# Kernel tuning notes

Hardware: AMD Instinct MI355X
Metric: run time of the kernel (lower is better)

## Reference

```python
import jax, jax.numpy as jnp
import numpy as np

B, M, D = 512, 100000, 256
EPS = 1e-8  # torch.cosine_similarity eps
TEMP = 10.0  # softmax temperature from source


def setup_inputs() -> dict:
    key = jax.random.key(0)
    kx, kk, kv = jax.random.split(key, 3)
    x = jax.random.normal(kx, (B, D), dtype=jnp.float32)
    memory_keys = jax.random.normal(kk, (M, D), dtype=jnp.float32) * 0.1
    memory_values = jax.random.normal(kv, (M, D), dtype=jnp.float32) * 0.1
    return {"x": x, "memory_keys": memory_keys, "memory_values": memory_values}


def reference(x, memory_keys, memory_values):
    # cosine similarity between x [B,D] and memory_keys [M,D] -> [B,M]
    dots = jnp.einsum("bd,md->bm", x, memory_keys)
    xn = jnp.linalg.norm(x, axis=-1)          # [B]
    kn = jnp.linalg.norm(memory_keys, axis=-1)  # [M]
    denom = jnp.maximum(xn[:, None] * kn[None, :], EPS)
    sims = dots / denom                         # [B,M]
    attn = jax.nn.softmax(sims * TEMP, axis=-1)  # [B,M]
    retrieved = jnp.einsum("bm,md->bd", attn, memory_values)  # [B,D]
    return retrieved, attn
```

## Files before the change

### kernel.cpp

```cpp
#include <hip/hip_runtime.h>
#include <hip/hip_bf16.h>


#define MCOLS 100000
#define MP    100032
#define DDIM  256
#define CHUNK 1792
#define NTFULL 28
#define NCHUNK 56
#define NSLOT 56
#define CHUNK1 832
#define NT1   26
#define NCH1  128
#define ATTN_OFF 131072
#define WS_RXN  0
#define WS_RKN  512
#define WS_RCPL 100512
#define WS_XB_BYTE   409600ull
#define WS_VT_BYTE   1048576ull
#define WS_PART_BYTE 52264960ull
#define WS_KB_BYTE   84246528ull
#define WS_KB_END    (WS_KB_BYTE + 2ull*(size_t)MCOLS*DDIM)

#define GLL(g, l) __builtin_amdgcn_global_load_lds( \
    (const __attribute__((address_space(1))) void*)(g), \
    (__attribute__((address_space(3))) void*)(l), 16, 0, 0)

typedef short short8 __attribute__((ext_vector_type(8)));
typedef float f32x4  __attribute__((ext_vector_type(4)));

static __device__ __forceinline__ unsigned short f2bfu(float f) {
  union { __hip_bfloat16 h; unsigned short u; } cv;
  cv.h = __float2bfloat16(f);
  return cv.u;
}
static __device__ __forceinline__ unsigned int pk2(float a, float b) {
  return (unsigned int)f2bfu(a) | ((unsigned int)f2bfu(b) << 16);
}
static __device__ __forceinline__ short8 pack8(float4 a, float4 b) {
  short8 r;
  r[0] = (short)f2bfu(a.x); r[1] = (short)f2bfu(a.y);
  r[2] = (short)f2bfu(a.z); r[3] = (short)f2bfu(a.w);
  r[4] = (short)f2bfu(b.x); r[5] = (short)f2bfu(b.y);
  r[6] = (short)f2bfu(b.z); r[7] = (short)f2bfu(b.w);
  return r;
}

__global__ void k0_xn(const float* __restrict__ x, float* __restrict__ ws) {
  const int b = blockIdx.x, t = threadIdx.x;
  const float v = x[b*DDIM + t];
  float s = v*v;
  #pragma unroll
  for (int mk = 1; mk <= 32; mk <<= 1) s += __shfl_xor(s, mk);
  __shared__ float ps[4];
  if ((t & 63) == 0) ps[t >> 6] = s;
  __syncthreads();
  const float tot = ps[0] + ps[1] + ps[2] + ps[3];
  const float r10 = 10.0f / fmaxf(sqrtf(tot), 1e-12f);
  if (t == 0) ws[WS_RXN + b] = r10;
  unsigned short* xbp = (unsigned short*)((char*)ws + WS_XB_BYTE);
  xbp[b*DDIM + t] = f2bfu(v * r10);
}

template<bool WRITEKB>
__global__ __launch_bounds__(256) void k0c_kn(const float* __restrict__ K,
                                              float* __restrict__ ws) {
  const int t = threadIdx.x;
  const int mg = blockIdx.x*64 + (t >> 2);
  const int qq = t & 3;
  if (mg >= MCOLS) return;
  const float* kp = K + (size_t)mg*DDIM + 64*qq;
  float4 buf[16];
  float ss = 0.f;
  #pragma unroll
  for (int j = 0; j < 16; ++j) {
    buf[j] = *(const float4*)(kp + 4*j);
    ss += buf[j].x*buf[j].x + buf[j].y*buf[j].y + buf[j].z*buf[j].z + buf[j].w*buf[j].w;
  }
  ss += __shfl_xor(ss, 1); ss += __shfl_xor(ss, 2);
  const float rk = 1.0f / fmaxf(sqrtf(ss), 1e-12f);
  if (qq == 0) ws[WS_RKN + mg] = rk;
  if (WRITEKB) {
    unsigned int* kb = (unsigned int*)((char*)ws + WS_KB_BYTE);
    #pragma unroll
    for (int j = 0; j < 8; ++j) {
      const float4 a = buf[2*j], b2 = buf[2*j+1];
      uint4 u;
      u.x = pk2(a.x*rk, a.y*rk);  u.y = pk2(a.z*rk, a.w*rk);
      u.z = pk2(b2.x*rk, b2.y*rk); u.w = pk2(b2.z*rk, b2.w*rk);
      const int slot = (8*qq + j) ^ (mg & 7);
      *(uint4*)(kb + (size_t)mg*128 + slot*4) = u;
    }
  }
}

__global__ __launch_bounds__(256) void k0b_tr(const float* __restrict__ V,
                                              float* __restrict__ ws) {
  const int t = threadIdx.x;
  const int m0 = blockIdx.x * 64;
  __shared__ float vt_f[64][261];
  #pragma unroll
  for (int i = 0; i < 4; ++i) {
    const int ml = (t >> 4) + 16*i;
    const int mg = m0 + ml;
    #pragma unroll
    for (int j = 0; j < 4; ++j) {
      const int d = 4*(t & 15) + 64*j;
      float4 v = make_float4(0.f, 0.f, 0.f, 0.f);
      if (mg < MCOLS) v = *(const float4*)(V + (size_t)mg*DDIM + d);
      vt_f[ml][d] = v.x; vt_f[ml][d+1] = v.y; vt_f[ml][d+2] = v.z; vt_f[ml][d+3] = v.w;
    }
  }
  __syncthreads();
  unsigned short* vt = (unsigned short*)((char*)ws + WS_VT_BYTE);
  const int tl = t & 15;
  const int s = tl >> 1, hf = tl & 1;
  const int mq = 8*s + 4*hf;
  #pragma unroll
  for (int it = 0; it < 16; ++it) {
    const int d = (t >> 4) + 16*it;
    uint2 u;
    u.x = pk2(vt_f[mq+0][d], vt_f[mq+1][d]);
    u.y = pk2(vt_f[mq+2][d], vt_f[mq+3][d]);
    const int sp = s ^ (d & 7);
    *(uint2*)(vt + (size_t)d*MP + m0 + sp*8 + 4*hf) = u;
  }
}

static __device__ __forceinline__ void stage_k(const char* __restrict__ kb,
                                               int m0, int w, int l,
                                               unsigned short (*klds)[256]) {
  #pragma unroll
  for (int i = 0; i < 4; ++i) {
    int r = m0 + w*8 + i*2 + (l >> 5);
    r = min(r, MCOLS - 1);
    const char* g = kb + (size_t)r*512 + (l & 31)*16;
    char* dst = (char*)&klds[w*8 + i*2][0];
    GLL(g, dst);
  }
}
static __device__ __forceinline__ void stage_k32(const char* __restrict__ kb,
                                                 int m0, int w, int l,
                                                 unsigned short (*klds)[256]) {
  #pragma unroll
  for (int i = 0; i < 2; ++i) {
    int r = m0 + w*4 + i*2 + (l >> 5);
    r = min(r, MCOLS - 1);
    const char* g = kb + (size_t)r*512 + (l & 31)*16;
    char* dst = (char*)&klds[w*4 + i*2][0];
    GLL(g, dst);
  }
}
static __device__ __forceinline__ void stage_vt(const char* __restrict__ vtb,
                                                int m1, int w, int l,
                                                unsigned short (*vtl)[64]) {
  #pragma unroll
  for (int i = 0; i < 4; ++i) {
    const int d = w*32 + i*8 + (l >> 3);
    const int ms = min(m1 + (l & 7)*8, MP - 8);
    const char* g = vtb + ((size_t)d*MP + ms)*2;
    char* dst = (char*)&vtl[w*32 + i*8][0];
    GLL(g, dst);
  }
}

__global__ __launch_bounds__(512, 8) void k1b_sum(const float* __restrict__ ws,
                                                  float* __restrict__ out) {
  const int bid = blockIdx.x;
  const int xg = bid & 7, i = bid >> 3;
  const int c = xg + 8*(i & 15), rb = i >> 4;
  const int t = threadIdx.x, w = t >> 6, l = t & 63, q = l >> 4, ln = l & 15;
  const int ar = w & 3, h = w >> 2, l7 = ln & 7;
  __shared__ __align__(16) unsigned short klds2[2][32][256];
  const char* kb = (const char*)ws + WS_KB_BYTE;
  const unsigned short* xb = (const unsigned short*)((const char*)ws + WS_XB_BYTE);
  const int R0 = rb*64;

  short8 xf[8];
  {
    const int row = R0 + 16*ar + ln;
    #pragma unroll
    for (int kk = 0; kk < 8; ++kk)
      xf[kk] = *(const short8*)(xb + row*DDIM + 32*kk + 8*q);
  }
  float lpr[4] = {0.f,0.f,0.f,0.f};
  const int mbase = c*CHUNK1;
  const int rem = MCOLS - mbase;
  const int nt = rem <= 0 ? 0 : min(NT1, (rem + 31) >> 5);

  if (nt > 0) {
    stage_k32(kb, mbase, w, l, klds2[0]);
    __syncthreads();
    for (int mt = 0; mt < nt; ++mt) {
      const int cur = mt & 1;
      const int m0 = mbase + mt*32;
      if (mt + 1 < nt) stage_k32(kb, m0 + 32, w, l, klds2[cur ^ 1]);
      const char* kbase = (const char*)&klds2[cur][0][0];
      const int row0 = 16*h + ln;
      f32x4 acc = {0.f,0.f,0.f,0.f};
      #pragma unroll
      for (int kk = 0; kk < 8; ++kk) {
        const int sl = ((q + 4*kk) ^ l7) << 4;
        const short8 b0 = *(const short8*)(kbase + row0*512 + sl);
        acc = __builtin_amdgcn_mfma_f32_16x16x32_bf16(xf[kk], b0, acc, 0,0,0);
      }
      const int mr = m0 + row0;
      const bool ok = mr < MCOLS;
      #pragma unroll
      for (int r = 0; r < 4; ++r)
        lpr[r] += ok ? __expf(acc[r]) : 0.f;
      __syncthreads();
    }
  }
  #pragma unroll
  for (int r = 0; r < 4; ++r) {
    float s = lpr[r];
    s += __shfl_xor(s, 1); s += __shfl_xor(s, 2);
    s += __shfl_xor(s, 4); s += __shfl_xor(s, 8);
    if (ln == 0)
      out[(size_t)(c*2 + h)*512 + R0 + 16*ar + 4*q + r] = s;
  }
}

template<int NSUM>
__global__ void k2_final(const float* __restrict__ out, float* __restrict__ ws) {
  const int b = blockIdx.x, t = threadIdx.x;
  float v = (t < NSUM) ? out[(size_t)t*512 + b] : 0.f;
  #pragma unroll
  for (int mk = 1; mk <= 32; mk <<= 1) v += __shfl_xor(v, mk);
  __shared__ float s2[4];
  if ((t & 63) == 0) s2[t >> 6] = v;
  __syncthreads();
  if (t == 0) ws[WS_RCPL + b] = 1.0f / (s2[0] + s2[1] + s2[2] + s2[3]);
}

__global__ __launch_bounds__(512, 4) void k3a_main(float* __restrict__ ws,
                                                   float* __restrict__ out) {
  const int bid = blockIdx.x;
  const int xg = bid & 7, i = bid >> 3;
  const int c = xg + 8*(i % 7), rb = i / 7;
  const int t = threadIdx.x, w = t >> 6, l = t & 63, q = l >> 4, ln = l & 15;
  const int ar = w & 3, h = w >> 2, l7 = ln & 7;
  __shared__ __align__(16) unsigned short klds[64][256];
  __shared__ __align__(16) unsigned short vtl[256][64];
  __shared__ __align__(16) unsigned short plds[64][64];
  const char* kb  = (const char*)ws + WS_KB_BYTE;
  const char* vtb = (const char*)ws + WS_VT_BYTE;
  const unsigned short* xb = (const unsigned short*)((const char*)ws + WS_XB_BYTE);
  const int R0 = rb*64;

  short8 xf[8];
  {
    const int row = R0 + 16*ar + ln;
    #pragma unroll
    for (int kk = 0; kk < 8; ++kk)
      xf[kk] = *(const short8*)(xb + row*DDIM + 32*kk + 8*q);
  }
  float rlq[4];
  #pragma unroll
  for (int r = 0; r < 4; ++r)
    rlq[r] = ws[WS_RCPL + R0 + 16*ar + 4*q + r];
  f32x4 apv[8];
  #pragma unroll
  for (int dx = 0; dx < 8; ++dx) { f32x4 z = {0.f,0.f,0.f,0.f}; apv[dx] = z; }
  const int d2 = 128*h;
  float* attn = out + ATTN_OFF;
  const int mbase = c*CHUNK;
  const int nt = min(NTFULL, (MCOLS - mbase + 63) >> 6);
  unsigned short* pf = &plds[0][0];

  stage_k(kb, mbase, w, l, klds);
  __syncthreads();

  for (int mt = 0; mt < nt; ++mt) {
    const int m0 = mbase + mt*64;
    stage_vt(vtb, m0, w, l, vtl);
    const int row0 = 32*h + ln;
    f32x4 acc[2];
    { f32x4 z = {0.f,0.f,0.f,0.f}; acc[0] = z; acc[1] = z; }
    #pragma unroll
    for (int kk = 0; kk < 8; ++kk) {
      const int sl = ((q + 4*kk) ^ l7) << 4;
      const short8 b0 = *(const short8*)((const char*)&klds[0][0] + row0*512 + sl);
      const short8 b1 = *(const short8*)((const char*)&klds[0][0] + (row0 + 16)*512 + sl);
      acc[0] = __builtin_amdgcn_mfma_f32_16x16x32_bf16(xf[kk], b0, acc[0], 0,0,0);
      acc[1] = __builtin_amdgcn_mfma_f32_16x16x32_bf16(xf[kk], b1, acc[1], 0,0,0);
    }
    const int mr0 = m0 + row0, mr1 = mr0 + 16;
    const bool ok0 = mr0 < MCOLS, ok1 = mr1 < MCOLS;
    #pragma unroll
    for (int r = 0; r < 4; ++r) {
      const int rowl = 16*ar + 4*q + r;
      const float p0v = ok0 ? __expf(acc[0][r]) : 0.f;
      const float p1v = ok1 ? __expf(acc[1][r]) : 0.f;
      float* arow = attn + (size_t)(R0 + rowl)*MCOLS;
      if (ok0) arow[mr0] = p0v*rlq[r];
      if (ok1) arow[mr1] = p1v*rlq[r];
      const int r7 = rowl & 7;
      pf[rowl*64 + ((((ln>>3) + 4*h    ) ^ r7) << 3) + (ln & 7)] = f2bfu(p0v);
      pf[rowl*64 + ((((ln>>3) + 4*h + 2) ^ r7) << 3) + (ln & 7)] = f2bfu(p1v);
    }
    __syncthreads();
    if (mt + 1 < nt) stage_k(kb, m0 + 64, w, l, klds);
    const int prow = 16*ar + ln;
    const short8 af0 = *(const short8*)(pf + prow*64 + ((q       ^ l7) << 3));
    const short8 af1 = *(const short8*)(pf + prow*64 + (((4 + q) ^ l7) << 3));
    #pragma unroll
    for (int dx = 0; dx < 8; ++dx) {
      const int R = d2 + 16*dx + ln;
      const char* vr = (const char*)&vtl[0][0] + R*128;
      const short8 bv0 = *(const short8*)(vr + ((q       ^ l7) << 4));
      const short8 bv1 = *(const short8*)(vr + (((4 + q) ^ l7) << 4));
      apv[dx] = __builtin_amdgcn_mfma_f32_16x16x32_bf16(af0, bv0, apv[dx], 0,0,0);
      apv[dx] = __builtin_amdgcn_mfma_f32_16x16x32_bf16(af1, bv1, apv[dx], 0,0,0);
    }
    __syncthreads();
  }

  float* part = (float*)((char*)ws + WS_PART_BYTE);
  #pragma unroll
  for (int dx = 0; dx < 8; ++dx)
    #pragma unroll
    for (int r = 0; r < 4; ++r)
      part[((size_t)c*512 + R0 + 16*ar + 4*q + r)*256 + d2 + 16*dx + ln]
        = apv[dx][r]*rlq[r];
}

static __device__ __forceinline__ void load_xf(const float* __restrict__ x,
                                               int brow0, int q, int ln,
                                               short8 xf[2][8]) {
  #pragma unroll
  for (int as = 0; as < 2; ++as) {
    const int row = brow0 + 16*as + ln;
    #pragma unroll
    for (int kk = 0; kk < 8; ++kk) {
      const float* p = x + row*DDIM + 32*kk + 8*q;
      xf[as][kk] = pack8(*(const float4*)p, *(const float4*)(p + 4));
    }
  }
}

__global__ __launch_bounds__(512, 2) void k3b_main(const float* __restrict__ x,
                                                   const float* __restrict__ K,
                                                   float* __restrict__ ws,
                                                   float* __restrict__ out) {
  const int bid = blockIdx.x;
  const int c = bid >> 2, rb = bid & 3;
  const int t = threadIdx.x, w = t >> 6, l = t & 63, q = l >> 4, ln = l & 15;
  const int h = w & 1, rg = w >> 1;
  __shared__ __align__(16) unsigned short plds[2][128][72];
  const int R0 = rb*128;
  short8 xf[2][8];
  const int brow0 = R0 + 32*rg;
  load_xf(x, brow0, q, ln, xf);
  float rxn[2][4];
  #pragma unroll
  for (int as = 0; as < 2; ++as)
    #pragma unroll
    for (int r = 0; r < 4; ++r)
      rxn[as][r] = ws[WS_RXN + brow0 + 16*as + 4*q + r];
  float lpr[2][4] = {{0.f,0.f,0.f,0.f},{0.f,0.f,0.f,0.f}};
  f32x4 apv[2][8];
  #pragma unroll
  for (int bs = 0; bs < 2; ++bs)
    #pragma unroll
    for (int dx = 0; dx < 8; ++dx) { f32x4 z = {0.f,0.f,0.f,0.f}; apv[bs][dx] = z; }
  const int b2 = 32*(w & 3), d2 = 128*(w >> 2);
  const unsigned short* vt = (const unsigned short*)((const char*)ws + WS_VT_BYTE);
  const float* rknw = ws + WS_RKN;
  float* attn = out + ATTN_OFF;
  const int mbase = c*CHUNK;
  const int nt = min(NTFULL, (MCOLS - mbase + 63) >> 6);
  const int l7 = ln & 7;

  for (int mt = 0; mt < nt; ++mt) {
    const int m0 = mbase + mt*64;
    const int mr0 = m0 + 32*h + ln, mr1 = mr0 + 16;
    const int kr0 = min(mr0, MCOLS-1), kr1 = min(mr1, MCOLS-1);
    f32x4 acc[2][2];
    #pragma unroll
    for (int as = 0; as < 2; ++as)
      #pragma unroll
      for (int mm = 0; mm < 2; ++mm) { f32x4 z = {0.f,0.f,0.f,0.f}; acc[as][mm] = z; }
    const float* p0 = K + (size_t)kr0*DDIM + 8*q;
    const float* p1 = K + (size_t)kr1*DDIM + 8*q;
    #pragma unroll
    for (int kk = 0; kk < 8; ++kk) {
      const short8 b0 = pack8(*(const float4*)(p0 + 32*kk), *(const float4*)(p0 + 32*kk + 4));
      const short8 b1 = pack8(*(const float4*)(p1 + 32*kk), *(const float4*)(p1 + 32*kk + 4));
      acc[0][0] = __builtin_amdgcn_mfma_f32_16x16x32_bf16(xf[0][kk], b0, acc[0][0], 0,0,0);
      acc[0][1] = __builtin_amdgcn_mfma_f32_16x16x32_bf16(xf[0][kk], b1, acc[0][1], 0,0,0);
      acc[1][0] = __builtin_amdgcn_mfma_f32_16x16x32_bf16(xf[1][kk], b0, acc[1][0], 0,0,0);
      acc[1][1] = __builtin_amdgcn_mfma_f32_16x16x32_bf16(xf[1][kk], b1, acc[1][1], 0,0,0);
    }
    const float rk0 = rknw[kr0], rk1 = rknw[kr1];
    const bool ok0 = mr0 < MCOLS, ok1 = mr1 < MCOLS;
    #pragma unroll
    for (int as = 0; as < 2; ++as)
      #pragma unroll
      for (int r = 0; r < 4; ++r) {
        const int rowl = 32*rg + 16*as + 4*q + r;
        const float p0v = ok0 ? __expf(acc[as][0][r]*rxn[as][r]*rk0) : 0.f;
        const float p1v = ok1 ? __expf(acc[as][1][r]*rxn[as][r]*rk1) : 0.f;
        float* arow = attn + (size_t)(R0 + rowl)*MCOLS;
        if (ok0) arow[mr0] = p0v;
        if (ok1) arow[mr1] = p1v;
        lpr[as][r] += p0v + p1v;
        plds[mt & 1][rowl][32*h + ln]      = f2bfu(p0v);
        plds[mt & 1][rowl][32*h + 16 + ln] = f2bfu(p1v);
      }
    __syncthreads();
    const unsigned short (*pb)[72] = plds[mt & 1];
    const short8 af00 = *(const short8*)&pb[b2 + ln][8*q];
    const short8 af01 = *(const short8*)&pb[b2 + ln][32 + 8*q];
    const short8 af10 = *(const short8*)&pb[b2 + 16 + ln][8*q];
    const short8 af11 = *(const short8*)&pb[b2 + 16 + ln][32 + 8*q];
    #pragma unroll
    for (int dx = 0; dx < 8; ++dx) {
      const int R = d2 + 16*dx + ln;
      const size_t rbase = (size_t)R*MP + m0;
      const short8 bv0 = *(const short8*)(vt + rbase + ((q     ^ (R & 7)) << 3));
      const short8 bv1 = *(const short8*)(vt + rbase + (((4+q) ^ (R & 7)) << 3));
      apv[0][dx] = __builtin_amdgcn_mfma_f32_16x16x32_bf16(af00, bv0, apv[0][dx], 0,0,0);
      apv[0][dx] = __builtin_amdgcn_mfma_f32_16x16x32_bf16(af01, bv1, apv[0][dx], 0,0,0);
      apv[1][dx] = __builtin_amdgcn_mfma_f32_16x16x32_bf16(af10, bv0, apv[1][dx], 0,0,0);
      apv[1][dx] = __builtin_amdgcn_mfma_f32_16x16x32_bf16(af11, bv1, apv[1][dx], 0,0,0);
    }
  }

  #pragma unroll
  for (int as = 0; as < 2; ++as)
    #pragma unroll
    for (int r = 0; r < 4; ++r) {
      float s = lpr[as][r];
      s += __shfl_xor(s, 1); s += __shfl_xor(s, 2);
      s += __shfl_xor(s, 4); s += __shfl_xor(s, 8);
      if (ln == 0)
        out[(size_t)(c*2 + h)*512 + brow0 + 16*as + 4*q + r] = s;
    }
  float* part = (float*)((char*)ws + WS_PART_BYTE);
  #pragma unroll
  for (int bs = 0; bs < 2; ++bs)
    #pragma unroll
    for (int dx = 0; dx < 8; ++dx)
      #pragma unroll
      for (int r = 0; r < 4; ++r)
        part[((size_t)c*512 + R0 + b2 + 16*bs + 4*q + r)*256 + d2 + 16*dx + ln]
          = apv[bs][dx][r];
}

template<bool NORM>
__global__ void k4_red(const float* __restrict__ ws, float* __restrict__ out) {
  const int b = blockIdx.x, t = threadIdx.x;
  const float* part = (const float*)((const char*)ws + WS_PART_BYTE);
  float acc = 0.f;
  for (int cc = 0; cc < NSLOT; ++cc)
    acc += part[((size_t)cc*512 + b)*256 + t];
  if (!NORM) acc *= ws[WS_RCPL + b];
  out[b*DDIM + t] = acc;
}

__global__ void k5_scale(const float* __restrict__ ws, float* __restrict__ out) {
  const int row = blockIdx.y;
  const int i4 = blockIdx.x*256 + threadIdx.x;
  if (i4 >= MCOLS/4) return;
  const float s = ws[WS_RCPL + row];
  float4* p = (float4*)(out + ATTN_OFF + (size_t)row*MCOLS) + i4;
  float4 v = *p;
  v.x *= s; v.y *= s; v.z *= s; v.w *= s;
  *p = v;
}

extern "C" void kernel_launch(void* const* d_in, const int* in_sizes, int n_in,
                              void* d_out, int out_size, void* d_ws, size_t ws_size,
                              hipStream_t stream) {
  const float* x = (const float*)d_in[0];
  const float* K = (const float*)d_in[1];
  const float* V = (const float*)d_in[2];
  float* out = (float*)d_out;
  float* ws  = (float*)d_ws;
  const bool useKB = ws_size >= WS_KB_END;

  k0_xn<<<512, 256, 0, stream>>>(x, ws);
  if (useKB) k0c_kn<true ><<<1563, 256, 0, stream>>>(K, ws);
  else       k0c_kn<false><<<1563, 256, 0, stream>>>(K, ws);
  k0b_tr<<<MP/64, 256, 0, stream>>>(V, ws);
  if (useKB) {
    k1b_sum<<<1024, 512, 0, stream>>>(ws, out);
    k2_final<256><<<512, 256, 0, stream>>>(out, ws);
    k3a_main<<<448, 512, 0, stream>>>(ws, out);
    k4_red<true><<<512, 256, 0, stream>>>(ws, out);
  } else {
    k3b_main<<<224, 512, 0, stream>>>(x, K, ws, out);
    k2_final<112><<<512, 256, 0, stream>>>(out, ws);
    k5_scale<<<dim3((MCOLS/4 + 255)/256, 512), 256, 0, stream>>>(ws, out);
    k4_red<false><<<512, 256, 0, stream>>>(ws, out);
  }
}
```

Measured before the change: 253.1 us.

## Fuse key normalization and bf16 conversion with softmax-denominator pass

Replaces the separate key-normalize/bf16-pack kernel and the k1b_sum exp-sum kernel with one fused kernel. Each block loads 64 key rows, normalizes them, writes the bf16 keys to workspace and LDS, then runs MFMA against all 512 x rows to produce partial exp sums per chunk. This avoids rereading the bf16 keys from global memory in a separate pass and removes one launch. The cost is a larger partial-sum reduction (1563 chunks) and reloading x fragments from global for every block. In the KB path the fused kernel no longer writes the per-key reciprocal norm (WS_RKN), which the before code stored there.

```diff
diff --git a/kernel.cpp b/kernel.cpp
--- a/kernel.cpp
+++ b/kernel.cpp
@@ -9,9 +9,8 @@
 #define NTFULL 28
 #define NCHUNK 56
 #define NSLOT 56
-#define CHUNK1 832
-#define NT1   26
-#define NCH1  128
+#define NCHA  1563
+#define PSTAT_OFF 50530816
 #define ATTN_OFF 131072
 #define WS_RXN  0
 #define WS_RKN  512
@@ -62,7 +61,94 @@
   xbp[b*DDIM + t] = f2bfu(v * r10);
 }
 
-template<bool WRITEKB>
+__global__ __launch_bounds__(512, 4) void kA_fused(const float* __restrict__ K,
+                                                   float* __restrict__ ws,
+                                                   float* __restrict__ out) {
+  const int c = blockIdx.x;
+  const int m0 = c*64;
+  const int t = threadIdx.x;
+  __shared__ __align__(16) unsigned short klds[64][264];
+  {
+    const int ml = t >> 3, tc = t & 7;
+    const int mg = m0 + ml;
+    const bool mok = mg < MCOLS;
+    const float* kp = K + (size_t)(mok ? mg : MCOLS-1)*DDIM + 32*tc;
+    float4 buf[8];
+    float ss = 0.f;
+    #pragma unroll
+    for (int j = 0; j < 8; ++j) {
+      buf[j] = *(const float4*)(kp + 4*j);
+      ss += buf[j].x*buf[j].x + buf[j].y*buf[j].y + buf[j].z*buf[j].z + buf[j].w*buf[j].w;
+    }
+    ss += __shfl_xor(ss, 1); ss += __shfl_xor(ss, 2); ss += __shfl_xor(ss, 4);
+    const float rk = mok ? (1.0f / fmaxf(sqrtf(ss), 1e-12f)) : 0.f;
+    unsigned int* kb = (unsigned int*)((char*)ws + WS_KB_BYTE);
+    #pragma unroll
+    for (int j = 0; j < 4; ++j) {
+      const float4 a = buf[2*j], b2 = buf[2*j+1];
+      uint4 u;
+      u.x = pk2(a.x*rk, a.y*rk);   u.y = pk2(a.z*rk, a.w*rk);
+      u.z = pk2(b2.x*rk, b2.y*rk); u.w = pk2(b2.z*rk, b2.w*rk);
+      const int slot = 4*tc + j;
+      if (mok) *(uint4*)(kb + (size_t)mg*128 + (slot ^ (ml & 7))*4) = u;
+      *(uint4*)&klds[ml][slot*8] = u;
+    }
+  }
+  __syncthreads();
+  const int w = t >> 6, l = t & 63, q = l >> 4, ln = l & 15;
+  const unsigned short* xb = (const unsigned short*)((const char*)ws + WS_XB_BYTE);
+  float* pst = out + PSTAT_OFF + (size_t)c*512;
+  #pragma unroll 1
+  for (int as = 0; as < 4; ++as) {
+    const int xrow = 64*w + 16*as + ln;
+    short8 xf[8];
+    #pragma unroll
+    for (int kk = 0; kk < 8; ++kk)
+      xf[kk] = *(const short8*)(xb + xrow*DDIM + 32*kk + 8*q);
+    f32x4 acc[4];
+    #pragma unroll
+    for (int mm = 0; mm < 4; ++mm) { f32x4 z = {0.f,0.f,0.f,0.f}; acc[mm] = z; }
+    #pragma unroll
+    for (int kk = 0; kk < 8; ++kk) {
+      #pragma unroll
+      for (int mm = 0; mm < 4; ++mm) {
+        const short8 b = *(const short8*)((const char*)&klds[0][0]
+                                          + (16*mm + ln)*528 + (4*kk + q)*16);
+        acc[mm] = __builtin_amdgcn_mfma_f32_16x16x32_bf16(xf[kk], b, acc[mm], 0,0,0);
+      }
+    }
+    float srow[4] = {0.f, 0.f, 0.f, 0.f};
+    #pragma unroll
+    for (int mm = 0; mm < 4; ++mm) {
+      const bool ok = (m0 + 16*mm + ln) < MCOLS;
+      #pragma unroll
+      for (int r = 0; r < 4; ++r)
+        srow[r] += ok ? __expf(acc[mm][r]) : 0.f;
+    }
+    #pragma unroll
+    for (int r = 0; r < 4; ++r) {
+      float s = srow[r];
+      s += __shfl_xor(s, 1); s += __shfl_xor(s, 2);
+      s += __shfl_xor(s, 4); s += __shfl_xor(s, 8);
+      if (ln == 0) pst[64*w + 16*as + 4*q + r] = s;
+    }
+  }
+}
+
+__global__ void k2A_final(const float* __restrict__ out, float* __restrict__ ws) {
+  const int b = blockIdx.x, t = threadIdx.x;
+  const float* pst = out + PSTAT_OFF;
+  float v = 0.f;
+  for (int ch = t; ch < NCHA; ch += 256)
+    v += pst[(size_t)ch*512 + b];
+  #pragma unroll
+  for (int mk = 1; mk <= 32; mk <<= 1) v += __shfl_xor(v, mk);
+  __shared__ float s2[4];
+  if ((t & 63) == 0) s2[t >> 6] = v;
+  __syncthreads();
+  if (t == 0) ws[WS_RCPL + b] = 1.0f / (s2[0] + s2[1] + s2[2] + s2[3]);
+}
+
 __global__ __launch_bounds__(256) void k0c_kn(const float* __restrict__ K,
                                               float* __restrict__ ws) {
   const int t = threadIdx.x;
@@ -70,28 +156,14 @@
   const int qq = t & 3;
   if (mg >= MCOLS) return;
   const float* kp = K + (size_t)mg*DDIM + 64*qq;
-  float4 buf[16];
   float ss = 0.f;
   #pragma unroll
   for (int j = 0; j < 16; ++j) {
-    buf[j] = *(const float4*)(kp + 4*j);
-    ss += buf[j].x*buf[j].x + buf[j].y*buf[j].y + buf[j].z*buf[j].z + buf[j].w*buf[j].w;
+    const float4 a = *(const float4*)(kp + 4*j);
+    ss += a.x*a.x + a.y*a.y + a.z*a.z + a.w*a.w;
   }
   ss += __shfl_xor(ss, 1); ss += __shfl_xor(ss, 2);
-  const float rk = 1.0f / fmaxf(sqrtf(ss), 1e-12f);
-  if (qq == 0) ws[WS_RKN + mg] = rk;
-  if (WRITEKB) {
-    unsigned int* kb = (unsigned int*)((char*)ws + WS_KB_BYTE);
-    #pragma unroll
-    for (int j = 0; j < 8; ++j) {
-      const float4 a = buf[2*j], b2 = buf[2*j+1];
-      uint4 u;
-      u.x = pk2(a.x*rk, a.y*rk);  u.y = pk2(a.z*rk, a.w*rk);
-      u.z = pk2(b2.x*rk, b2.y*rk); u.w = pk2(b2.z*rk, b2.w*rk);
-      const int slot = (8*qq + j) ^ (mg & 7);
-      *(uint4*)(kb + (size_t)mg*128 + slot*4) = u;
-    }
-  }
+  if (qq == 0) ws[WS_RKN + mg] = 1.0f / fmaxf(sqrtf(ss), 1e-12f);
 }
 
 __global__ __launch_bounds__(256) void k0b_tr(const float* __restrict__ V,
@@ -139,18 +211,6 @@
     GLL(g, dst);
   }
 }
-static __device__ __forceinline__ void stage_k32(const char* __restrict__ kb,
-                                                 int m0, int w, int l,
-                                                 unsigned short (*klds)[256]) {
-  #pragma unroll
-  for (int i = 0; i < 2; ++i) {
-    int r = m0 + w*4 + i*2 + (l >> 5);
-    r = min(r, MCOLS - 1);
-    const char* g = kb + (size_t)r*512 + (l & 31)*16;
-    char* dst = (char*)&klds[w*4 + i*2][0];
-    GLL(g, dst);
-  }
-}
 static __device__ __forceinline__ void stage_vt(const char* __restrict__ vtb,
                                                 int m1, int w, int l,
                                                 unsigned short (*vtl)[64]) {
@@ -161,64 +221,6 @@
     const char* g = vtb + ((size_t)d*MP + ms)*2;
     char* dst = (char*)&vtl[w*32 + i*8][0];
     GLL(g, dst);
-  }
-}
-
-__global__ __launch_bounds__(512, 8) void k1b_sum(const float* __restrict__ ws,
-                                                  float* __restrict__ out) {
-  const int bid = blockIdx.x;
-  const int xg = bid & 7, i = bid >> 3;
-  const int c = xg + 8*(i & 15), rb = i >> 4;
-  const int t = threadIdx.x, w = t >> 6, l = t & 63, q = l >> 4, ln = l & 15;
-  const int ar = w & 3, h = w >> 2, l7 = ln & 7;
-  __shared__ __align__(16) unsigned short klds2[2][32][256];
-  const char* kb = (const char*)ws + WS_KB_BYTE;
-  const unsigned short* xb = (const unsigned short*)((const char*)ws + WS_XB_BYTE);
-  const int R0 = rb*64;
-
-  short8 xf[8];
-  {
-    const int row = R0 + 16*ar + ln;
-    #pragma unroll
-    for (int kk = 0; kk < 8; ++kk)
-      xf[kk] = *(const short8*)(xb + row*DDIM + 32*kk + 8*q);
-  }
-  float lpr[4] = {0.f,0.f,0.f,0.f};
-  const int mbase = c*CHUNK1;
-  const int rem = MCOLS - mbase;
-  const int nt = rem <= 0 ? 0 : min(NT1, (rem + 31) >> 5);
-
-  if (nt > 0) {
-    stage_k32(kb, mbase, w, l, klds2[0]);
-    __syncthreads();
-    for (int mt = 0; mt < nt; ++mt) {
-      const int cur = mt & 1;
-      const int m0 = mbase + mt*32;
-      if (mt + 1 < nt) stage_k32(kb, m0 + 32, w, l, klds2[cur ^ 1]);
-      const char* kbase = (const char*)&klds2[cur][0][0];
-      const int row0 = 16*h + ln;
-      f32x4 acc = {0.f,0.f,0.f,0.f};
-      #pragma unroll
-      for (int kk = 0; kk < 8; ++kk) {
-        const int sl = ((q + 4*kk) ^ l7) << 4;
-        const short8 b0 = *(const short8*)(kbase + row0*512 + sl);
-        acc = __builtin_amdgcn_mfma_f32_16x16x32_bf16(xf[kk], b0, acc, 0,0,0);
-      }
-      const int mr = m0 + row0;
-      const bool ok = mr < MCOLS;
-      #pragma unroll
-      for (int r = 0; r < 4; ++r)
-        lpr[r] += ok ? __expf(acc[r]) : 0.f;
-      __syncthreads();
-    }
-  }
-  #pragma unroll
-  for (int r = 0; r < 4; ++r) {
-    float s = lpr[r];
-    s += __shfl_xor(s, 1); s += __shfl_xor(s, 2);
-    s += __shfl_xor(s, 4); s += __shfl_xor(s, 8);
-    if (ln == 0)
-      out[(size_t)(c*2 + h)*512 + R0 + 16*ar + 4*q + r] = s;
   }
 }
 
@@ -482,15 +484,15 @@
   const bool useKB = ws_size >= WS_KB_END;
 
   k0_xn<<<512, 256, 0, stream>>>(x, ws);
-  if (useKB) k0c_kn<true ><<<1563, 256, 0, stream>>>(K, ws);
-  else       k0c_kn<false><<<1563, 256, 0, stream>>>(K, ws);
-  k0b_tr<<<MP/64, 256, 0, stream>>>(V, ws);
   if (useKB) {
-    k1b_sum<<<1024, 512, 0, stream>>>(ws, out);
-    k2_final<256><<<512, 256, 0, stream>>>(out, ws);
+    kA_fused<<<NCHA, 512, 0, stream>>>(K, ws, out);
+    k0b_tr<<<MP/64, 256, 0, stream>>>(V, ws);
+    k2A_final<<<512, 256, 0, stream>>>(out, ws);
     k3a_main<<<448, 512, 0, stream>>>(ws, out);
     k4_red<true><<<512, 256, 0, stream>>>(ws, out);
   } else {
+    k0c_kn<<<1563, 256, 0, stream>>>(K, ws);
+    k0b_tr<<<MP/64, 256, 0, stream>>>(V, ws);
     k3b_main<<<224, 512, 0, stream>>>(x, K, ws, out);
     k2_final<112><<<512, 256, 0, stream>>>(out, ws);
     k5_scale<<<dim3((MCOLS/4 + 255)/256, 512), 256, 0, stream>>>(ws, out);
```

Result: slower. 354.3 us (+40.0%).

## Stage probabilities as fp32 in LDS for coalesced attn stores and reschedule V staging

Applied to the files above, without the earlier changes.

The exp'd probabilities are now kept as fp32 in a swizzled LDS tile, and the attn output is written from there as float4 row-contiguous stores instead of scattered scalar stores from MFMA layout. The A operands for the PV MFMA are repacked to bf16 from that fp32 tile. V-tile staging moves to after the PV step, prefetching the next tile, with explicit waitcnt and barriers replacing __syncthreads. The aim is to coalesce the large attn write stream and overlap loads with compute. In exchange it doubles the LDS used for P and adds an extra barrier per iteration.

```diff
diff --git a/kernel.cpp b/kernel.cpp
--- a/kernel.cpp
+++ b/kernel.cpp
@@ -11,7 +11,6 @@
 #define NSLOT 56
 #define CHUNK1 832
 #define NT1   26
-#define NCH1  128
 #define ATTN_OFF 131072
 #define WS_RXN  0
 #define WS_RKN  512
@@ -243,7 +242,7 @@
   const int ar = w & 3, h = w >> 2, l7 = ln & 7;
   __shared__ __align__(16) unsigned short klds[64][256];
   __shared__ __align__(16) unsigned short vtl[256][64];
-  __shared__ __align__(16) unsigned short plds[64][64];
+  __shared__ __align__(16) float pf32[64][64];
   const char* kb  = (const char*)ws + WS_KB_BYTE;
   const char* vtb = (const char*)ws + WS_VT_BYTE;
   const unsigned short* xb = (const unsigned short*)((const char*)ws + WS_XB_BYTE);
@@ -260,6 +259,9 @@
   #pragma unroll
   for (int r = 0; r < 4; ++r)
     rlq[r] = ws[WS_RCPL + R0 + 16*ar + 4*q + r];
+  const int sr0 = 8*w + (l >> 4);
+  const float srlq0 = ws[WS_RCPL + R0 + sr0];
+  const float srlq1 = ws[WS_RCPL + R0 + sr0 + 4];
   f32x4 apv[8];
   #pragma unroll
   for (int dx = 0; dx < 8; ++dx) { f32x4 z = {0.f,0.f,0.f,0.f}; apv[dx] = z; }
@@ -267,14 +269,16 @@
   float* attn = out + ATTN_OFF;
   const int mbase = c*CHUNK;
   const int nt = min(NTFULL, (MCOLS - mbase + 63) >> 6);
-  unsigned short* pf = &plds[0][0];
 
   stage_k(kb, mbase, w, l, klds);
-  __syncthreads();
+  stage_vt(vtb, mbase, w, l, vtl);
+  asm volatile("s_waitcnt vmcnt(0) lgkmcnt(0)" ::: "memory");
+  __builtin_amdgcn_sched_barrier(0);
+  __builtin_amdgcn_s_barrier();
+  __builtin_amdgcn_sched_barrier(0);
 
   for (int mt = 0; mt < nt; ++mt) {
     const int m0 = mbase + mt*64;
-    stage_vt(vtb, m0, w, l, vtl);
     const int row0 = 32*h + ln;
     f32x4 acc[2];
     { f32x4 z = {0.f,0.f,0.f,0.f}; acc[0] = z; acc[1] = z; }
@@ -293,18 +297,40 @@
       const int rowl = 16*ar + 4*q + r;
       const float p0v = ok0 ? __expf(acc[0][r]) : 0.f;
       const float p1v = ok1 ? __expf(acc[1][r]) : 0.f;
-      float* arow = attn + (size_t)(R0 + rowl)*MCOLS;
-      if (ok0) arow[mr0] = p0v*rlq[r];
-      if (ok1) arow[mr1] = p1v*rlq[r];
       const int r7 = rowl & 7;
-      pf[rowl*64 + ((((ln>>3) + 4*h    ) ^ r7) << 3) + (ln & 7)] = f2bfu(p0v);
-      pf[rowl*64 + ((((ln>>3) + 4*h + 2) ^ r7) << 3) + (ln & 7)] = f2bfu(p1v);
-    }
-    __syncthreads();
+      pf32[rowl][(((8*h + (ln >> 2))    ) ^ r7)*4 + (ln & 3)] = p0v;
+      pf32[rowl][(((8*h + 4 + (ln >> 2))) ^ r7)*4 + (ln & 3)] = p1v;
+    }
+    asm volatile("s_waitcnt vmcnt(0) lgkmcnt(0)" ::: "memory");
+    __builtin_amdgcn_sched_barrier(0);
+    __builtin_amdgcn_s_barrier();
+    __builtin_amdgcn_sched_barrier(0);
     if (mt + 1 < nt) stage_k(kb, m0 + 64, w, l, klds);
-    const int prow = 16*ar + ln;
-    const short8 af0 = *(const short8*)(pf + prow*64 + ((q       ^ l7) << 3));
-    const short8 af1 = *(const short8*)(pf + prow*64 + (((4 + q) ^ l7) << 3));
+    __builtin_amdgcn_sched_barrier(0);
+    {
+      const int c4 = l & 15;
+      const bool cok = (m0 + 4*c4) < MCOLS;
+      const int rowA = sr0, rowB = sr0 + 4;
+      const float4 va = *(const float4*)&pf32[rowA][(c4 ^ (rowA & 7))*4];
+      const float4 vb = *(const float4*)&pf32[rowB][(c4 ^ (rowB & 7))*4];
+      if (cok) {
+        float4 o;
+        o.x = va.x*srlq0; o.y = va.y*srlq0; o.z = va.z*srlq0; o.w = va.w*srlq0;
+        *(float4*)(attn + (size_t)(R0 + rowA)*MCOLS + m0 + 4*c4) = o;
+        o.x = vb.x*srlq1; o.y = vb.y*srlq1; o.z = vb.z*srlq1; o.w = vb.w*srlq1;
+        *(float4*)(attn + (size_t)(R0 + rowB)*MCOLS + m0 + 4*c4) = o;
+      }
+    }
+    short8 af0, af1;
+    {
+      const int prow = 16*ar + ln, p7 = prow & 7;
+      const float4 a0 = *(const float4*)&pf32[prow][((2*q    ) ^ p7)*4];
+      const float4 a1 = *(const float4*)&pf32[prow][((2*q + 1) ^ p7)*4];
+      const float4 a2 = *(const float4*)&pf32[prow][((8 + 2*q) ^ p7)*4];
+      const float4 a3 = *(const float4*)&pf32[prow][((9 + 2*q) ^ p7)*4];
+      af0 = pack8(a0, a1);
+      af1 = pack8(a2, a3);
+    }
     #pragma unroll
     for (int dx = 0; dx < 8; ++dx) {
       const int R = d2 + 16*dx + ln;
@@ -314,7 +340,14 @@
       apv[dx] = __builtin_amdgcn_mfma_f32_16x16x32_bf16(af0, bv0, apv[dx], 0,0,0);
       apv[dx] = __builtin_amdgcn_mfma_f32_16x16x32_bf16(af1, bv1, apv[dx], 0,0,0);
     }
-    __syncthreads();
+    __builtin_amdgcn_sched_barrier(0);
+    __builtin_amdgcn_s_barrier();
+    __builtin_amdgcn_sched_barrier(0);
+    if (mt + 1 < nt) stage_vt(vtb, m0 + 64, w, l, vtl);
+    asm volatile("s_waitcnt vmcnt(6)" ::: "memory");
+    __builtin_amdgcn_sched_barrier(0);
+    __builtin_amdgcn_s_barrier();
+    __builtin_amdgcn_sched_barrier(0);
   }
 
   float* part = (float*)((char*)ws + WS_PART_BYTE);
```

After: 282.6 us. +11.7%, slower.
